# Performance work log

Measured on AMD Instinct MI355X. Metric: run time of the kernel, lower is better.

The kernel has to match this reference:

```python
import jax, jax.numpy as jnp
import numpy as np

N_NODES = 10000
N_EDGES = 320000
NODE_F = 64
EDGE_F = 32
H = 256
L = 6
HEADS = 8
OUT = H // HEADS
N_GRAPHS = 16
NEG_SLOPE = 0.2  # PyG GATConv leaky_relu slope


def setup_inputs() -> dict:
    key = jax.random.key(0)
    ks = jax.random.split(key, 32)
    s = 0.05
    f32 = jnp.float32
    inp = {}
    inp["x"] = jax.random.normal(ks[0], (N_NODES, NODE_F), f32)
    inp["edge_index"] = jax.random.randint(ks[1], (2, N_EDGES), 0, N_NODES)
    inp["edge_attr"] = jax.random.normal(ks[2], (N_EDGES, EDGE_F), f32)
    inp["batch"] = jnp.sort(jax.random.randint(ks[3], (N_NODES,), 0, N_GRAPHS))
    # embeddings
    inp["node_w"] = jax.random.normal(ks[4], (H, NODE_F), f32) * s
    inp["node_b"] = jnp.zeros((H,), f32)
    inp["edge_emb_w"] = jax.random.normal(ks[5], (H, EDGE_F), f32) * s
    inp["edge_emb_b"] = jnp.zeros((H,), f32)
    # stacked GATConv params (shared lin for src/dst since in_channels is int)
    inp["lin_w"] = jax.random.normal(ks[6], (L, H, H), f32) * s
    inp["att_src"] = jax.random.normal(ks[7], (L, HEADS, OUT), f32) * s
    inp["att_dst"] = jax.random.normal(ks[8], (L, HEADS, OUT), f32) * s
    inp["att_edge"] = jax.random.normal(ks[9], (L, HEADS, OUT), f32) * s
    inp["lin_edge_w"] = jax.random.normal(ks[10], (L, H, H), f32) * s
    inp["conv_b"] = jnp.zeros((L, H), f32)
    inp["ln_g"] = jnp.ones((L, H), f32)
    inp["ln_b"] = jnp.zeros((L, H), f32)
    # MLP heads: Linear(2H->H), Linear(H->H/2), Linear(H/2->3)
    inp["pw1"] = jax.random.normal(ks[11], (H, 2 * H), f32) * s
    inp["pb1"] = jnp.zeros((H,), f32)
    inp["pw2"] = jax.random.normal(ks[12], (H // 2, H), f32) * s
    inp["pb2"] = jnp.zeros((H // 2,), f32)
    inp["pw3"] = jax.random.normal(ks[13], (3, H // 2), f32) * s
    inp["pb3"] = jnp.zeros((3,), f32)
    inp["mw1"] = jax.random.normal(ks[14], (H, 2 * H), f32) * s
    inp["mb1"] = jnp.zeros((H,), f32)
    inp["mw2"] = jax.random.normal(ks[15], (H // 2, H), f32) * s
    inp["mb2"] = jnp.zeros((H // 2,), f32)
    inp["mw3"] = jax.random.normal(ks[16], (3, H // 2), f32) * s
    inp["mb3"] = jnp.zeros((3,), f32)
    return inp


def _ln(x, g, b):
    mu = jnp.mean(x, -1, keepdims=True)
    var = jnp.mean(jnp.square(x - mu), -1, keepdims=True)
    return g * (x - mu) * jax.lax.rsqrt(var + 1e-5) + b


def _mlp(z, w1, b1, w2, b2, w3, b3):
    h = jax.nn.gelu(z @ w1.T + b1, approximate=False)
    h = jax.nn.gelu(h @ w2.T + b2, approximate=False)
    return jax.nn.sigmoid(h @ w3.T + b3)


def _gnn_forward(x, edge_attr, src, dst, batch,
                 node_w, node_b, edge_emb_w, edge_emb_b,
                 lin_w, att_src, att_dst, att_edge, lin_edge_w, conv_b,
                 ln_g, ln_b,
                 pw1, pb1, pw2, pb2, pw3, pb3,
                 mw1, mb1, mw2, mb2, mw3, mb3):
    h = x @ node_w.T + node_b                       # [N, H]
    ea = edge_attr @ edge_emb_w.T + edge_emb_b      # [E, H]
    # PyG add_self_loops(fill_value='mean'): loop attr = mean of incoming edge attrs
    cnt = jax.ops.segment_sum(jnp.ones((N_EDGES,), h.dtype), dst, N_NODES)
    loop_attr = jax.ops.segment_sum(ea, dst, N_NODES) / jnp.maximum(cnt, 1.0)[:, None]
    ea_full = jnp.concatenate([ea, loop_attr], 0)   # [E+N, H]
    loops = jnp.arange(N_NODES, dtype=src.dtype)
    src_f = jnp.concatenate([src, loops])
    dst_f = jnp.concatenate([dst, loops])
    for i in range(L):
        x_in = h
        xw = (h @ lin_w[i].T).reshape(N_NODES, HEADS, OUT)
        eap = (ea_full @ lin_edge_w[i].T).reshape(-1, HEADS, OUT)
        a_src = jnp.sum(xw * att_src[i], -1)        # [N, heads]
        a_dst = jnp.sum(xw * att_dst[i], -1)
        alpha = a_src[src_f] + a_dst[dst_f] + jnp.sum(eap * att_edge[i], -1)  # [E+N, heads]
        alpha = jnp.where(alpha > 0, alpha, NEG_SLOPE * alpha)
        amax = jax.ops.segment_max(alpha, dst_f, N_NODES)
        e = jnp.exp(alpha - amax[dst_f])
        denom = jax.ops.segment_sum(e, dst_f, N_NODES)
        w = e / (denom[dst_f] + 1e-16)
        msg = xw[src_f] * w[:, :, None]             # [E+N, heads, out]
        hi = jax.ops.segment_sum(msg, dst_f, N_NODES).reshape(N_NODES, H) + conv_b[i]
        hi = jax.nn.gelu(_ln(hi, ln_g[i], ln_b[i]), approximate=False)
        h = hi + x_in if i > 0 else hi
    sums = jax.ops.segment_sum(h, batch, N_GRAPHS)  # [G, H]
    ncnt = jax.ops.segment_sum(jnp.ones((N_NODES,), h.dtype), batch, N_GRAPHS)
    mean = sums / jnp.maximum(ncnt, 1.0)[:, None]
    xg = jnp.concatenate([mean, sums], 1)           # [G, 2H]
    params = _mlp(xg, pw1, pb1, pw2, pb2, pw3, pb3)
    metrics = _mlp(xg, mw1, mb1, mw2, mb2, mw3, mb3)
    return params, metrics


def reference(x, edge_index, edge_attr, batch,
              node_w, node_b, edge_emb_w, edge_emb_b,
              lin_w, att_src, att_dst, att_edge, lin_edge_w, conv_b,
              ln_g, ln_b,
              pw1, pb1, pw2, pb2, pw3, pb3,
              mw1, mb1, mw2, mb2, mw3, mb3):
    return _gnn_forward(x, edge_attr, edge_index[0], edge_index[1], batch,
                        node_w, node_b, edge_emb_w, edge_emb_b,
                        lin_w, att_src, att_dst, att_edge, lin_edge_w, conv_b,
                        ln_g, ln_b,
                        pw1, pb1, pw2, pb2, pw3, pb3,
                        mw1, mb1, mw2, mb2, mw3, mb3)
```

## Files before the change

### kernel.cpp

```cpp
#include <hip/hip_runtime.h>
#include <math.h>

#define NN 10000
#define NE 320000
#define NODE_F 64
#define EDGE_F 32
#define HDIM 256
#define HEADS 8
#define LAYERS 6
#define NG 16
#define NPB 2
#define NOUT 48
#define LOG2E 1.4426950408889634f

typedef __attribute__((ext_vector_type(8))) short short8;
typedef __attribute__((ext_vector_type(4))) float float4v;
typedef __attribute__((ext_vector_type(2))) float floatx2;

__global__ void count_kernel(const int* __restrict__ dst, int* __restrict__ cnt) {
    int e = blockIdx.x * 256 + threadIdx.x;
    if (e < NE) atomicAdd(&cnt[dst[e]], 1);
}

__global__ void scan_kernel(const int* __restrict__ cnt, int* __restrict__ row_ptr,
                            int* __restrict__ pos) {
    __shared__ int wsum[16];
    __shared__ int woff[16];
    int t = threadIdx.x;
    int lane = t & 63, wid = t >> 6;
    const int chunk = 10;
    int lo = t * chunk;
    int loc[10];
    int s = 0;
    #pragma unroll
    for (int k = 0; k < 10; ++k) {
        int i = lo + k;
        int v = (i < NN) ? cnt[i] : 0;
        loc[k] = v;
        s += v;
    }
    int inc = s;
    #pragma unroll
    for (int off = 1; off < 64; off <<= 1) {
        int v = __shfl_up(inc, off, 64);
        if (lane >= off) inc += v;
    }
    if (lane == 63) wsum[wid] = inc;
    __syncthreads();
    if (t < 16) {
        int inc2 = wsum[t];
        #pragma unroll
        for (int off = 1; off < 16; off <<= 1) {
            int u = __shfl_up(inc2, off, 16);
            if (t >= off) inc2 += u;
        }
        woff[t] = inc2;
    }
    __syncthreads();
    int base = inc - s + (wid ? woff[wid - 1] : 0);
    #pragma unroll
    for (int k = 0; k < 10; ++k) {
        int i = lo + k;
        if (i < NN) {
            row_ptr[i] = base;
            pos[i] = base;
            base += loc[k];
        }
    }
    if (t == 1023) row_ptr[NN] = woff[15];
}

__global__ void scatter_kernel(const int* __restrict__ src, const int* __restrict__ dst,
                               int* __restrict__ pos, int2* __restrict__ csr_se) {
    int e = blockIdx.x * 256 + threadIdx.x;
    if (e >= NE) return;
    int d = dst[e];
    int idx = atomicAdd(&pos[d], 1);
    csr_se[idx] = make_int2(src[e], e);
}

__device__ __forceinline__ ushort f2bf(float f) {
    union { float f; unsigned u; } v; v.f = f;
    unsigned u = v.u;
    return (ushort)((u + 0x7fffu + ((u >> 16) & 1u)) >> 16);
}
__device__ __forceinline__ float bf2f(ushort b) {
    union { unsigned u; float f; } v; v.u = ((unsigned)b) << 16; return v.f;
}

__global__ __launch_bounds__(256) void prep_kernel(const float* __restrict__ att_edge,
                                                   const float* __restrict__ lin_edge_w,
                                                   const float* __restrict__ eew,
                                                   const float* __restrict__ eeb,
                                                   ushort* __restrict__ webbf,
                                                   float* __restrict__ bebuf) {
    int ih = blockIdx.x;
    int i = ih >> 3, h = ih & 7;
    __shared__ float vsh[HDIM];
    int t = threadIdx.x;
    float s = 0.f;
    const float* ae = att_edge + ih * 32;
    const float* lw = lin_edge_w + ((size_t)i * HDIM + h * 32) * HDIM + t;
    #pragma unroll
    for (int o = 0; o < 32; ++o) s += ae[o] * lw[(size_t)o * HDIM];
    vsh[t] = s;
    __syncthreads();
    if (t < EDGE_F) {
        float acc = 0.f;
        for (int k = 0; k < HDIM; ++k) acc += vsh[k] * eew[k * EDGE_F + t];
        webbf[ih * EDGE_F + t] = f2bf(acc * LOG2E);
    } else if (t == EDGE_F) {
        float acc = 0.f;
        for (int k = 0; k < HDIM; ++k) acc += vsh[k] * eeb[k];
        bebuf[ih] = acc * LOG2E;
    }
}

__global__ __launch_bounds__(256) void preE_kernel(const float* __restrict__ edge_attr,
                                                   const ushort* __restrict__ web,
                                                   const float* __restrict__ be,
                                                   ushort* __restrict__ preEb) {
    int wv = threadIdx.x >> 6, l = threadIdx.x & 63;
    int base = blockIdx.x * 64 + wv * 16;
    int m = l & 15, kq = (l >> 4) * 8;
    const float* ar = edge_attr + (size_t)(base + m) * EDGE_F + kq;
    float4 a0 = *(const float4*)(ar);
    float4 a1 = *(const float4*)(ar + 4);
    short8 afrag;
    afrag[0] = (short)f2bf(a0.x); afrag[1] = (short)f2bf(a0.y);
    afrag[2] = (short)f2bf(a0.z); afrag[3] = (short)f2bf(a0.w);
    afrag[4] = (short)f2bf(a1.x); afrag[5] = (short)f2bf(a1.y);
    afrag[6] = (short)f2bf(a1.z); afrag[7] = (short)f2bf(a1.w);
    float4v zero = {0.f, 0.f, 0.f, 0.f};
    float4v acc[3];
    #pragma unroll
    for (int ct = 0; ct < 3; ++ct) {
        short8 bfrag = *(const short8*)(web + (size_t)(ct * 16 + m) * EDGE_F + kq);
        acc[ct] = __builtin_amdgcn_mfma_f32_16x16x32_bf16(afrag, bfrag, zero, 0, 0, 0);
    }
    #pragma unroll
    for (int ct = 0; ct < 3; ++ct) {
        int oc = ct * 16 + m;
        int li = oc >> 3, hh = oc & 7;
        float bv = be[oc];
        #pragma unroll
        for (int r = 0; r < 4; ++r) {
            int row = (l >> 4) * 4 + r;
            preEb[(size_t)li * NE * 8 + (size_t)(base + row) * 8 + hh] = f2bf(acc[ct][r] + bv);
        }
    }
}

__global__ void tobf_all_kernel(const float* __restrict__ lin_w, const float* __restrict__ node_w,
                                const float* __restrict__ x, ushort* __restrict__ wbhi,
                                ushort* __restrict__ nwhi, ushort* __restrict__ xhi) {
    const int N1 = LAYERS * HDIM * HDIM;
    const int N2 = N1 + HDIM * NODE_F;
    const int N3 = N2 + NN * NODE_F;
    int i = blockIdx.x * 256 + threadIdx.x;
    if (i < N1) wbhi[i] = f2bf(lin_w[i]);
    else if (i < N2) nwhi[i - N1] = f2bf(node_w[i - N1]);
    else if (i < N3) xhi[i - N2] = f2bf(x[i - N2]);
}

__global__ __launch_bounds__(128) void gemm_bf1(const ushort* __restrict__ Ah,
                                                const ushort* __restrict__ Bh,
                                                const float* __restrict__ bias,
                                                float* __restrict__ C,
                                                ushort* __restrict__ Chi,
                                                unsigned char* __restrict__ Cf8,
                                                const float* __restrict__ att_s,
                                                const float* __restrict__ att_d,
                                                float* __restrict__ a_src,
                                                float* __restrict__ a_dst,
                                                int N, int K, int J) {
    __shared__ ushort sAh[64][40], sBh[64][40];
    int nb = blockIdx.y * 64, jb = blockIdx.x * 64;
    int t = threadIdx.x, w = t >> 6, l = t & 63;
    int srow = t >> 1, sq = (t & 1) * 16;
    int fr = l & 15, fq = (l >> 4) * 8;
    float4v acc[2][4] = {};
    for (int kt = 0; kt < K; kt += 32) {
        int gr = nb + srow;
        short8 a0 = {0,0,0,0,0,0,0,0}, a1 = {0,0,0,0,0,0,0,0};
        if (gr < N) {
            const short8* pa = (const short8*)(Ah + (size_t)gr * K + kt + sq);
            a0 = pa[0]; a1 = pa[1];
        }
        *(short8*)&sAh[srow][sq] = a0; *(short8*)&sAh[srow][sq + 8] = a1;
        const short8* pb = (const short8*)(Bh + (size_t)(jb + srow) * K + kt + sq);
        short8 b0 = pb[0], b1 = pb[1];
        *(short8*)&sBh[srow][sq] = b0; *(short8*)&sBh[srow][sq + 8] = b1;
        __syncthreads();
        short8 bh[4];
        #pragma unroll
        for (int nt = 0; nt < 4; ++nt)
            bh[nt] = *(const short8*)&sBh[nt * 16 + fr][fq];
        #pragma unroll
        for (int mt = 0; mt < 2; ++mt) {
            short8 ah = *(const short8*)&sAh[w * 32 + mt * 16 + fr][fq];
            #pragma unroll
            for (int nt = 0; nt < 4; ++nt)
                acc[mt][nt] = __builtin_amdgcn_mfma_f32_16x16x32_bf16(ah, bh[nt], acc[mt][nt], 0, 0, 0);
        }
        __syncthreads();
    }
    #pragma unroll
    for (int mt = 0; mt < 2; ++mt) {
        #pragma unroll
        for (int nt = 0; nt < 4; ++nt) {
            int col = jb + nt * 16 + fr;
            float bv = bias ? bias[col] : 0.f;
            #pragma unroll
            for (int r = 0; r < 4; ++r) {
                int row = nb + w * 32 + mt * 16 + (l >> 4) * 4 + r;
                if (row < N) {
                    float v = acc[mt][nt][r] + bv;
                    if (C) C[(size_t)row * J + col] = v;
                    if (Chi) Chi[(size_t)row * J + col] = f2bf(v);
                    if (Cf8) {
                        int pk8 = __builtin_amdgcn_cvt_pk_fp8_f32(v, v, 0, false);
                        Cf8[(size_t)row * J + col] = (unsigned char)(pk8 & 0xff);
                    }
                }
            }
        }
    }
    if (att_s) {
        int head0 = jb >> 5;
        float cs[4], cd[4];
        #pragma unroll
        for (int nt = 0; nt < 4; ++nt) {
            cs[nt] = att_s[jb + nt * 16 + fr] * LOG2E;
            cd[nt] = att_d[jb + nt * 16 + fr] * LOG2E;
        }
        #pragma unroll
        for (int mt = 0; mt < 2; ++mt) {
            #pragma unroll
            for (int r = 0; r < 4; ++r) {
                float s0 = acc[mt][0][r] * cs[0] + acc[mt][1][r] * cs[1];
                float s1 = acc[mt][2][r] * cs[2] + acc[mt][3][r] * cs[3];
                float d0 = acc[mt][0][r] * cd[0] + acc[mt][1][r] * cd[1];
                float d1 = acc[mt][2][r] * cd[2] + acc[mt][3][r] * cd[3];
                #pragma unroll
                for (int off = 8; off >= 1; off >>= 1) {
                    s0 += __shfl_xor(s0, off, 16);
                    s1 += __shfl_xor(s1, off, 16);
                    d0 += __shfl_xor(d0, off, 16);
                    d1 += __shfl_xor(d1, off, 16);
                }
                if (fr == 0) {
                    int row = nb + w * 32 + mt * 16 + (l >> 4) * 4 + r;
                    if (row < N) {
                        a_src[row * 8 + head0]     = s0;
                        a_src[row * 8 + head0 + 1] = s1;
                        a_dst[row * 8 + head0]     = d0;
                        a_dst[row * 8 + head0 + 1] = d1;
                    }
                }
            }
        }
    }
}

__device__ __forceinline__ float gelu_exact(float x) {
    return 0.5f * x * (1.f + erff(x * 0.70710678118654752f));
}

__global__ __launch_bounds__(64 * NPB) void node_kernel(const unsigned char* __restrict__ xwf8,
                                                  const ushort* __restrict__ pb,
                                                  const float* __restrict__ a_src,
                                                  const float* __restrict__ a_dst,
                                                  const int* __restrict__ row_ptr,
                                                  const int2* __restrict__ csr_se,
                                                  const float* __restrict__ h_prev,
                                                  float* __restrict__ h_next,
                                                  ushort* __restrict__ hhi,
                                                  const float* __restrict__ cb,
                                                  const float* __restrict__ lg,
                                                  const float* __restrict__ lb, int first) {
    int wv = threadIdx.x >> 6, l = threadIdx.x & 63;
    int n = blockIdx.x * NPB + wv;
    int start = row_ptr[n], end = row_ptr[n + 1];
    int hc = l >> 3;
    int hc8 = l & 56;
    int jj = l & 7;
    float adnh = a_dst[n * 8 + hc];
    const unsigned char* xb = xwf8 + 4 * l;

    float den = 0.f, acc[4] = {0.f, 0.f, 0.f, 0.f};
    float psum = 0.f;
    for (int idx = start; idx < end; idx += 8) {
        int myi = idx + jj;
        bool valid = myi < end;
        int2 se = valid ? csr_se[myi] : make_int2(n, 0);
        int snj[8];
        #pragma unroll
        for (int j = 0; j < 8; ++j) snj[j] = __shfl(se.x, hc8 + j, 64);
        unsigned g[8];
        #pragma unroll
        for (int j = 0; j < 8; ++j) g[j] = *(const unsigned*)(xb + (size_t)snj[j] * HDIM);
        float w_t = 0.f;
        if (valid) {
            float p_t = bf2f(pb[(size_t)se.y * 8 + hc]);
            float a_t = a_src[(size_t)se.x * 8 + hc] + adnh + p_t;
            w_t = exp2f(fminf(fmaxf(a_t, 0.2f * a_t), 57.7f));
            psum += p_t;
        }
        #pragma unroll
        for (int j = 0; j < 8; ++j) {
            float wj = __shfl(w_t, hc8 + j, 64);
            floatx2 lo = __builtin_amdgcn_cvt_pk_f32_fp8(g[j], false);
            floatx2 hi = __builtin_amdgcn_cvt_pk_f32_fp8(g[j], true);
            den += wj;
            acc[0] += wj * lo.x;
            acc[1] += wj * lo.y;
            acc[2] += wj * hi.x;
            acc[3] += wj * hi.y;
        }
    }
    #pragma unroll
    for (int off = 1; off < 8; off <<= 1) psum += __shfl_xor(psum, off, 64);
    int deg = end - start;
    float preLv = deg > 0 ? psum / (float)deg : 0.f;
    {
        float al = a_src[n * 8 + hc] + adnh + preLv;
        al = fminf(fmaxf(al, 0.2f * al), 57.7f);
        float wself = exp2f(al);
        den += wself;
        unsigned gs = *(const unsigned*)(xb + (size_t)n * HDIM);
        floatx2 lo = __builtin_amdgcn_cvt_pk_f32_fp8(gs, false);
        floatx2 hi = __builtin_amdgcn_cvt_pk_f32_fp8(gs, true);
        acc[0] += wself * lo.x;
        acc[1] += wself * lo.y;
        acc[2] += wself * hi.x;
        acc[3] += wself * hi.y;
    }
    float4 cb4 = *(const float4*)(cb + 4 * l);
    float invh = 1.f / (den + 1e-16f);
    acc[0] = acc[0] * invh + cb4.x;
    acc[1] = acc[1] * invh + cb4.y;
    acc[2] = acc[2] * invh + cb4.z;
    acc[3] = acc[3] * invh + cb4.w;

    float part = acc[0] + acc[1] + acc[2] + acc[3];
    #pragma unroll
    for (int off = 32; off >= 1; off >>= 1) part += __shfl_xor(part, off, 64);
    float mu = part * (1.f / 256.f);
    float p2 = 0.f;
    #pragma unroll
    for (int j = 0; j < 4; ++j) {
        float d = acc[j] - mu;
        p2 += d * d;
    }
    #pragma unroll
    for (int off = 32; off >= 1; off >>= 1) p2 += __shfl_xor(p2, off, 64);
    float rstd = rsqrtf(p2 * (1.f / 256.f) + 1e-5f);

    float4 lg4 = *(const float4*)(lg + 4 * l);
    float4 lb4 = *(const float4*)(lb + 4 * l);
    float o4[4];
    float lgv[4] = {lg4.x, lg4.y, lg4.z, lg4.w};
    float lbv[4] = {lb4.x, lb4.y, lb4.z, lb4.w};
    float4 hp = make_float4(0.f, 0.f, 0.f, 0.f);
    if (!first) hp = *(const float4*)(h_prev + (size_t)n * HDIM + 4 * l);
    float hpv[4] = {hp.x, hp.y, hp.z, hp.w};
    #pragma unroll
    for (int j = 0; j < 4; ++j) {
        float y = (acc[j] - mu) * rstd * lgv[j] + lbv[j];
        o4[j] = gelu_exact(y) + hpv[j];
    }
    *(float4*)(h_next + (size_t)n * HDIM + 4 * l) = make_float4(o4[0], o4[1], o4[2], o4[3]);
    if (hhi) {
        uint2 ph;
        ph.x = (unsigned)f2bf(o4[0]) | ((unsigned)f2bf(o4[1]) << 16);
        ph.y = (unsigned)f2bf(o4[2]) | ((unsigned)f2bf(o4[3]) << 16);
        *(uint2*)(hhi + (size_t)n * HDIM + 4 * l) = ph;
    }
}

__global__ __launch_bounds__(256) void graph_sum_kernel(const float* __restrict__ h,
                                                        const int* __restrict__ batch,
                                                        float* __restrict__ sums) {
    int t = threadIdx.x;
    int n0 = blockIdx.x * 64;
    int n1 = min(NN, n0 + 64);
    float acc = 0.f;
    int cur = batch[n0];
    for (int n = n0; n < n1; ++n) {
        int b = batch[n];
        if (b != cur) {
            atomicAdd(&sums[cur * HDIM + t], acc);
            acc = 0.f;
            cur = b;
        }
        acc += h[(size_t)n * HDIM + t];
    }
    atomicAdd(&sums[cur * HDIM + t], acc);
}

__device__ __forceinline__ int lower_bound_dev(const int* a, int n, int v) {
    int lo = 0, hi = n;
    while (lo < hi) {
        int mid = (lo + hi) >> 1;
        if (a[mid] < v) lo = mid + 1; else hi = mid;
    }
    return lo;
}

__global__ __launch_bounds__(256) void mlp_kernel(const float* __restrict__ sums,
                                                  const int* __restrict__ batch,
                                                  const float* __restrict__ pw1,
                                                  const float* __restrict__ pb1,
                                                  const float* __restrict__ pw2,
                                                  const float* __restrict__ pb2,
                                                  const float* __restrict__ pw3,
                                                  const float* __restrict__ pb3,
                                                  const float* __restrict__ mw1,
                                                  const float* __restrict__ mb1,
                                                  const float* __restrict__ mw2,
                                                  const float* __restrict__ mb2,
                                                  const float* __restrict__ mw3,
                                                  const float* __restrict__ mb3,
                                                  float* __restrict__ out) {
    int g = blockIdx.x, which = blockIdx.y;
    const float* w1 = which ? mw1 : pw1; const float* b1 = which ? mb1 : pb1;
    const float* w2 = which ? mw2 : pw2; const float* b2 = which ? mb2 : pb2;
    const float* w3 = which ? mw3 : pw3; const float* b3 = which ? mb3 : pb3;
    __shared__ float xg[512];
    __shared__ float h1[256];
    __shared__ float h2[128];
    __shared__ float cinv_s;
    int t = threadIdx.x;
    if (t == 0) {
        int s0 = lower_bound_dev(batch, NN, g), s1 = lower_bound_dev(batch, NN, g + 1);
        cinv_s = 1.f / fmaxf((float)(s1 - s0), 1.f);
    }
    __syncthreads();
    float sv = sums[g * HDIM + t];
    xg[t] = sv * cinv_s;
    xg[256 + t] = sv;
    __syncthreads();
    {
        const float* wr = w1 + (size_t)t * 512;
        float acc = 0.f;
        #pragma unroll 8
        for (int k = 0; k < 512; k += 4) {
            float4 wv = *(const float4*)(wr + k);
            acc += wv.x * xg[k] + wv.y * xg[k + 1] + wv.z * xg[k + 2] + wv.w * xg[k + 3];
        }
        h1[t] = gelu_exact(acc + b1[t]);
    }
    __syncthreads();
    {
        int row = t >> 1, hf = t & 1;
        const float* wr = w2 + (size_t)row * 256 + hf * 128;
        const float* hx = h1 + hf * 128;
        float acc = 0.f;
        #pragma unroll 8
        for (int k = 0; k < 128; k += 4) {
            float4 wv = *(const float4*)(wr + k);
            acc += wv.x * hx[k] + wv.y * hx[k + 1] + wv.z * hx[k + 2] + wv.w * hx[k + 3];
        }
        acc += __shfl_xor(acc, 1, 64);
        if (hf == 0) h2[row] = gelu_exact(acc + b2[row]);
    }
    __syncthreads();
    if (t < 64) {
        float v0 = h2[t], v1 = h2[64 + t];
        #pragma unroll
        for (int o = 0; o < 3; ++o) {
            float p = w3[o * 128 + t] * v0 + w3[o * 128 + 64 + t] * v1;
            #pragma unroll
            for (int off = 32; off >= 1; off >>= 1) p += __shfl_xor(p, off, 64);
            if (t == 0) out[which * (NG * 3) + g * 3 + o] = 1.f / (1.f + expf(-(p + b3[o])));
        }
    }
}

extern "C" void kernel_launch(void* const* d_in, const int* in_sizes, int n_in, void* d_out,
                              int out_size, void* d_ws, size_t ws_size, hipStream_t stream) {
    const float* x         = (const float*)d_in[0];
    const int*   ei        = (const int*)d_in[1];
    const int*   src       = ei;
    const int*   dst       = ei + NE;
    const float* edge_attr = (const float*)d_in[2];
    const int*   batch     = (const int*)d_in[3];
    const float* node_w    = (const float*)d_in[4];
    const float* node_b    = (const float*)d_in[5];
    const float* eew       = (const float*)d_in[6];
    const float* eeb       = (const float*)d_in[7];
    const float* lin_w     = (const float*)d_in[8];
    const float* att_src   = (const float*)d_in[9];
    const float* att_dst   = (const float*)d_in[10];
    const float* att_edge  = (const float*)d_in[11];
    const float* lin_edge_w= (const float*)d_in[12];
    const float* conv_b    = (const float*)d_in[13];
    const float* ln_g      = (const float*)d_in[14];
    const float* ln_b      = (const float*)d_in[15];
    const float* pw1 = (const float*)d_in[16]; const float* pb1 = (const float*)d_in[17];
    const float* pw2 = (const float*)d_in[18]; const float* pb2 = (const float*)d_in[19];
    const float* pw3 = (const float*)d_in[20]; const float* pb3 = (const float*)d_in[21];
    const float* mw1 = (const float*)d_in[22]; const float* mb1 = (const float*)d_in[23];
    const float* mw2 = (const float*)d_in[24]; const float* mb2 = (const float*)d_in[25];
    const float* mw3 = (const float*)d_in[26]; const float* mb3 = (const float*)d_in[27];
    float* out = (float*)d_out;

    float* wsf = (float*)d_ws;
    float* hA        = wsf; wsf += (size_t)NN * HDIM;
    float* hB        = wsf; wsf += (size_t)NN * HDIM;
    float* a_src     = wsf; wsf += (size_t)NN * HEADS;
    float* a_dst     = wsf; wsf += (size_t)NN * HEADS;
    float* bebuf     = wsf; wsf += 64;
    ushort* ubuf = (ushort*)wsf;
    ushort* preEb = ubuf; ubuf += (size_t)NE * NOUT;
    ushort* webbf = ubuf; ubuf += (size_t)NOUT * EDGE_F;
    ushort* hhi  = ubuf; ubuf += (size_t)NN * HDIM;
    unsigned char* xwf8 = (unsigned char*)ubuf; ubuf += (size_t)NN * HDIM / 2;
    ushort* wbhi = ubuf; ubuf += (size_t)LAYERS * HDIM * HDIM;
    ushort* xhi  = ubuf; ubuf += (size_t)NN * NODE_F;
    ushort* nwhi = ubuf; ubuf += (size_t)HDIM * NODE_F;
    int* ibuf    = (int*)ubuf;
    int* cnt     = ibuf; ibuf += NN + 16;
    float* sums  = (float*)ibuf; ibuf += NG * HDIM;
    int* row_ptr = ibuf; ibuf += NN + 16;
    int* pos     = ibuf; ibuf += NN + 16;
    ibuf += (((size_t)ibuf & 4) ? 1 : 0);
    int2* csr_se = (int2*)ibuf; ibuf += 2 * NE;

    hipMemsetAsync(cnt, 0, (NN + 16 + NG * HDIM) * sizeof(int), stream);
    count_kernel<<<(NE + 255) / 256, 256, 0, stream>>>(dst, cnt);
    scan_kernel<<<1, 1024, 0, stream>>>(cnt, row_ptr, pos);
    scatter_kernel<<<(NE + 255) / 256, 256, 0, stream>>>(src, dst, pos, csr_se);

    prep_kernel<<<LAYERS * HEADS, 256, 0, stream>>>(att_edge, lin_edge_w, eew, eeb, webbf, bebuf);
    preE_kernel<<<NE / 64, 256, 0, stream>>>(edge_attr, webbf, bebuf, preEb);

    {
        const int total = LAYERS * HDIM * HDIM + HDIM * NODE_F + NN * NODE_F;
        tobf_all_kernel<<<(total + 255) / 256, 256, 0, stream>>>(lin_w, node_w, x,
                                                                 wbhi, nwhi, xhi);
    }

    {
        dim3 grid(HDIM / 64, (NN + 63) / 64);
        gemm_bf1<<<grid, 128, 0, stream>>>(xhi, nwhi, node_b, nullptr, hhi, nullptr,
                                           nullptr, nullptr, nullptr, nullptr,
                                           NN, NODE_F, HDIM);
    }

    float* cur = hA;
    float* nxt = hB;
    for (int i = 0; i < LAYERS; ++i) {
        dim3 grid(HDIM / 64, (NN + 63) / 64);
        gemm_bf1<<<grid, 128, 0, stream>>>(hhi, wbhi + (size_t)i * HDIM * HDIM, nullptr,
                                           nullptr, nullptr, xwf8,
                                           att_src + i * HEADS * 32, att_dst + i * HEADS * 32,
                                           a_src, a_dst, NN, HDIM, HDIM);
        node_kernel<<<NN / NPB, 64 * NPB, 0, stream>>>(
            xwf8, preEb + (size_t)i * NE * 8, a_src, a_dst,
            row_ptr, csr_se, cur, nxt, (i == LAYERS - 1) ? nullptr : hhi,
            conv_b + i * HDIM, ln_g + i * HDIM, ln_b + i * HDIM, i == 0 ? 1 : 0);
        float* tmp = cur; cur = nxt; nxt = tmp;
    }

    graph_sum_kernel<<<(NN + 63) / 64, 256, 0, stream>>>(cur, batch, sums);
    {
        dim3 gm(NG, 2);
        mlp_kernel<<<gm, 256, 0, stream>>>(sums, batch, pw1, pb1, pw2, pb2, pw3, pb3,
                                           mw1, mb1, mw2, mb2, mw3, mb3, out);
    }
}
```

Measured before the change: 509.1 us.

## Unroll edge gather loop by 16 and fuse graph pooling into last node kernel

The per-node attention aggregation loop now handles two groups of 8 edges per iteration. This issues 16 fp8 row gathers before any arithmetic, so more memory loads are in flight per wave. In the last layer, the node kernel atomically adds its outputs into per-graph sums instead of writing h. That removes the separate graph_sum kernel and one full read of the hidden state. The trade-off is more register pressure in the unrolled loop and heavy float atomic contention on 16 graph rows, plus a non-deterministic summation order.

```diff
diff --git a/kernel.cpp b/kernel.cpp
--- a/kernel.cpp
+++ b/kernel.cpp
@@ -278,7 +278,9 @@
                                                   ushort* __restrict__ hhi,
                                                   const float* __restrict__ cb,
                                                   const float* __restrict__ lg,
-                                                  const float* __restrict__ lb, int first) {
+                                                  const float* __restrict__ lb, int first,
+                                                  const int* __restrict__ batch,
+                                                  float* __restrict__ sums) {
     int wv = threadIdx.x >> 6, l = threadIdx.x & 63;
     int n = blockIdx.x * NPB + wv;
     int start = row_ptr[n], end = row_ptr[n + 1];
@@ -290,28 +292,52 @@
 
     float den = 0.f, acc[4] = {0.f, 0.f, 0.f, 0.f};
     float psum = 0.f;
-    for (int idx = start; idx < end; idx += 8) {
-        int myi = idx + jj;
-        bool valid = myi < end;
-        int2 se = valid ? csr_se[myi] : make_int2(n, 0);
-        int snj[8];
-        #pragma unroll
-        for (int j = 0; j < 8; ++j) snj[j] = __shfl(se.x, hc8 + j, 64);
-        unsigned g[8];
-        #pragma unroll
-        for (int j = 0; j < 8; ++j) g[j] = *(const unsigned*)(xb + (size_t)snj[j] * HDIM);
-        float w_t = 0.f;
-        if (valid) {
-            float p_t = bf2f(pb[(size_t)se.y * 8 + hc]);
-            float a_t = a_src[(size_t)se.x * 8 + hc] + adnh + p_t;
-            w_t = exp2f(fminf(fmaxf(a_t, 0.2f * a_t), 57.7f));
+    for (int idx = start; idx < end; idx += 16) {
+        int myi0 = idx + jj;
+        int myi1 = idx + 8 + jj;
+        bool v0 = myi0 < end;
+        bool v1 = myi1 < end;
+        int2 se0 = v0 ? csr_se[myi0] : make_int2(n, 0);
+        int2 se1 = v1 ? csr_se[myi1] : make_int2(n, 0);
+        int snj0[8], snj1[8];
+        #pragma unroll
+        for (int j = 0; j < 8; ++j) snj0[j] = __shfl(se0.x, hc8 + j, 64);
+        #pragma unroll
+        for (int j = 0; j < 8; ++j) snj1[j] = __shfl(se1.x, hc8 + j, 64);
+        unsigned g0[8], g1[8];
+        #pragma unroll
+        for (int j = 0; j < 8; ++j) g0[j] = *(const unsigned*)(xb + (size_t)snj0[j] * HDIM);
+        #pragma unroll
+        for (int j = 0; j < 8; ++j) g1[j] = *(const unsigned*)(xb + (size_t)snj1[j] * HDIM);
+        float w0 = 0.f, w1 = 0.f;
+        if (v0) {
+            float p_t = bf2f(pb[(size_t)se0.y * 8 + hc]);
+            float a_t = a_src[(size_t)se0.x * 8 + hc] + adnh + p_t;
+            w0 = exp2f(fminf(fmaxf(a_t, 0.2f * a_t), 57.7f));
             psum += p_t;
         }
+        if (v1) {
+            float p_t = bf2f(pb[(size_t)se1.y * 8 + hc]);
+            float a_t = a_src[(size_t)se1.x * 8 + hc] + adnh + p_t;
+            w1 = exp2f(fminf(fmaxf(a_t, 0.2f * a_t), 57.7f));
+            psum += p_t;
+        }
         #pragma unroll
         for (int j = 0; j < 8; ++j) {
-            float wj = __shfl(w_t, hc8 + j, 64);
-            floatx2 lo = __builtin_amdgcn_cvt_pk_f32_fp8(g[j], false);
-            floatx2 hi = __builtin_amdgcn_cvt_pk_f32_fp8(g[j], true);
+            float wj = __shfl(w0, hc8 + j, 64);
+            floatx2 lo = __builtin_amdgcn_cvt_pk_f32_fp8(g0[j], false);
+            floatx2 hi = __builtin_amdgcn_cvt_pk_f32_fp8(g0[j], true);
+            den += wj;
+            acc[0] += wj * lo.x;
+            acc[1] += wj * lo.y;
+            acc[2] += wj * hi.x;
+            acc[3] += wj * hi.y;
+        }
+        #pragma unroll
+        for (int j = 0; j < 8; ++j) {
+            float wj = __shfl(w1, hc8 + j, 64);
+            floatx2 lo = __builtin_amdgcn_cvt_pk_f32_fp8(g1[j], false);
+            floatx2 hi = __builtin_amdgcn_cvt_pk_f32_fp8(g1[j], true);
             den += wj;
             acc[0] += wj * lo.x;
             acc[1] += wj * lo.y;
@@ -370,33 +396,22 @@
         float y = (acc[j] - mu) * rstd * lgv[j] + lbv[j];
         o4[j] = gelu_exact(y) + hpv[j];
     }
-    *(float4*)(h_next + (size_t)n * HDIM + 4 * l) = make_float4(o4[0], o4[1], o4[2], o4[3]);
+    if (sums) {
+        int b = batch[n];
+        float* sp = sums + (size_t)b * HDIM + 4 * l;
+        atomicAdd(sp + 0, o4[0]);
+        atomicAdd(sp + 1, o4[1]);
+        atomicAdd(sp + 2, o4[2]);
+        atomicAdd(sp + 3, o4[3]);
+    } else {
+        *(float4*)(h_next + (size_t)n * HDIM + 4 * l) = make_float4(o4[0], o4[1], o4[2], o4[3]);
+    }
     if (hhi) {
         uint2 ph;
         ph.x = (unsigned)f2bf(o4[0]) | ((unsigned)f2bf(o4[1]) << 16);
         ph.y = (unsigned)f2bf(o4[2]) | ((unsigned)f2bf(o4[3]) << 16);
         *(uint2*)(hhi + (size_t)n * HDIM + 4 * l) = ph;
     }
-}
-
-__global__ __launch_bounds__(256) void graph_sum_kernel(const float* __restrict__ h,
-                                                        const int* __restrict__ batch,
-                                                        float* __restrict__ sums) {
-    int t = threadIdx.x;
-    int n0 = blockIdx.x * 64;
-    int n1 = min(NN, n0 + 64);
-    float acc = 0.f;
-    int cur = batch[n0];
-    for (int n = n0; n < n1; ++n) {
-        int b = batch[n];
-        if (b != cur) {
-            atomicAdd(&sums[cur * HDIM + t], acc);
-            acc = 0.f;
-            cur = b;
-        }
-        acc += h[(size_t)n * HDIM + t];
-    }
-    atomicAdd(&sums[cur * HDIM + t], acc);
 }
 
 __device__ __forceinline__ int lower_bound_dev(const int* a, int n, int v) {
@@ -525,7 +540,6 @@
     float* sums  = (float*)ibuf; ibuf += NG * HDIM;
     int* row_ptr = ibuf; ibuf += NN + 16;
     int* pos     = ibuf; ibuf += NN + 16;
-    ibuf += (((size_t)ibuf & 4) ? 1 : 0);
     int2* csr_se = (int2*)ibuf; ibuf += 2 * NE;
 
     hipMemsetAsync(cnt, 0, (NN + 16 + NG * HDIM) * sizeof(int), stream);
@@ -557,14 +571,15 @@
                                            nullptr, nullptr, xwf8,
                                            att_src + i * HEADS * 32, att_dst + i * HEADS * 32,
                                            a_src, a_dst, NN, HDIM, HDIM);
+        int last = (i == LAYERS - 1);
         node_kernel<<<NN / NPB, 64 * NPB, 0, stream>>>(
             xwf8, preEb + (size_t)i * NE * 8, a_src, a_dst,
-            row_ptr, csr_se, cur, nxt, (i == LAYERS - 1) ? nullptr : hhi,
-            conv_b + i * HDIM, ln_g + i * HDIM, ln_b + i * HDIM, i == 0 ? 1 : 0);
+            row_ptr, csr_se, cur, nxt, last ? nullptr : hhi,
+            conv_b + i * HDIM, ln_g + i * HDIM, ln_b + i * HDIM, i == 0 ? 1 : 0,
+            batch, last ? sums : nullptr);
         float* tmp = cur; cur = nxt; nxt = tmp;
     }
 
-    graph_sum_kernel<<<(NN + 63) / 64, 256, 0, stream>>>(cur, batch, sums);
     {
         dim3 gm(NG, 2);
         mlp_kernel<<<gm, 256, 0, stream>>>(sums, batch, pw1, pb1, pw2, pb2, pw3, pb3,
```

Measured after the change: 629.0 us. 1.24x slower.

## Fold node embedding into first GAT linear and keep hidden state in bf16

Applied to the files above, without the earlier changes.

Precomputes the product of the first layer's lin_w with the node embedding weight and bias, so layer 0's projection runs as one K=64 GEMM straight from x and the separate embedding GEMM is dropped. The hidden state is also kept only in bf16 ping-pong buffers instead of fp32 plus a bf16 copy. This cuts fp32 reads and writes of the residual in every node_kernel and in graph_sum. The cost is lower residual precision, since bf16 rounding accumulates across layers.

```diff
diff --git a/kernel.cpp b/kernel.cpp
--- a/kernel.cpp
+++ b/kernel.cpp
@@ -114,6 +114,26 @@
         for (int k = 0; k < HDIM; ++k) acc += vsh[k] * eeb[k];
         bebuf[ih] = acc * LOG2E;
     }
+}
+
+__global__ __launch_bounds__(64) void fold0_kernel(const float* __restrict__ lin_w,
+                                                   const float* __restrict__ node_w,
+                                                   const float* __restrict__ node_b,
+                                                   ushort* __restrict__ w0p,
+                                                   float* __restrict__ b0p) {
+    int j = blockIdx.x, f = threadIdx.x;
+    const float* wr = lin_w + (size_t)j * HDIM;
+    float acc = 0.f, accb = 0.f;
+    for (int k = 0; k < HDIM; ++k) acc += wr[k] * node_w[k * NODE_F + f];
+    #pragma unroll
+    for (int m = 0; m < 4; ++m) {
+        int k = f + 64 * m;
+        accb += wr[k] * node_b[k];
+    }
+    w0p[j * NODE_F + f] = f2bf(acc);
+    #pragma unroll
+    for (int off = 32; off >= 1; off >>= 1) accb += __shfl_xor(accb, off, 64);
+    if (f == 0) b0p[j] = accb;
 }
 
 __global__ __launch_bounds__(256) void preE_kernel(const float* __restrict__ edge_attr,
@@ -151,29 +171,25 @@
     }
 }
 
-__global__ void tobf_all_kernel(const float* __restrict__ lin_w, const float* __restrict__ node_w,
+__global__ void tobf_all_kernel(const float* __restrict__ lin_w,
                                 const float* __restrict__ x, ushort* __restrict__ wbhi,
-                                ushort* __restrict__ nwhi, ushort* __restrict__ xhi) {
+                                ushort* __restrict__ xhi) {
     const int N1 = LAYERS * HDIM * HDIM;
-    const int N2 = N1 + HDIM * NODE_F;
-    const int N3 = N2 + NN * NODE_F;
+    const int N2 = N1 + NN * NODE_F;
     int i = blockIdx.x * 256 + threadIdx.x;
     if (i < N1) wbhi[i] = f2bf(lin_w[i]);
-    else if (i < N2) nwhi[i - N1] = f2bf(node_w[i - N1]);
-    else if (i < N3) xhi[i - N2] = f2bf(x[i - N2]);
+    else if (i < N2) xhi[i - N1] = f2bf(x[i - N1]);
 }
 
 __global__ __launch_bounds__(128) void gemm_bf1(const ushort* __restrict__ Ah,
                                                 const ushort* __restrict__ Bh,
                                                 const float* __restrict__ bias,
-                                                float* __restrict__ C,
-                                                ushort* __restrict__ Chi,
                                                 unsigned char* __restrict__ Cf8,
                                                 const float* __restrict__ att_s,
                                                 const float* __restrict__ att_d,
                                                 float* __restrict__ a_src,
                                                 float* __restrict__ a_dst,
-                                                int N, int K, int J) {
+                                                int N, int K) {
     __shared__ ushort sAh[64][40], sBh[64][40];
     int nb = blockIdx.y * 64, jb = blockIdx.x * 64;
     int t = threadIdx.x, w = t >> 6, l = t & 63;
@@ -205,28 +221,33 @@
         }
         __syncthreads();
     }
+    if (bias) {
+        #pragma unroll
+        for (int nt = 0; nt < 4; ++nt) {
+            float bv = bias[jb + nt * 16 + fr];
+            #pragma unroll
+            for (int mt = 0; mt < 2; ++mt)
+                #pragma unroll
+                for (int r = 0; r < 4; ++r) acc[mt][nt][r] += bv;
+        }
+    }
     #pragma unroll
     for (int mt = 0; mt < 2; ++mt) {
         #pragma unroll
         for (int nt = 0; nt < 4; ++nt) {
             int col = jb + nt * 16 + fr;
-            float bv = bias ? bias[col] : 0.f;
             #pragma unroll
             for (int r = 0; r < 4; ++r) {
                 int row = nb + w * 32 + mt * 16 + (l >> 4) * 4 + r;
                 if (row < N) {
-                    float v = acc[mt][nt][r] + bv;
-                    if (C) C[(size_t)row * J + col] = v;
-                    if (Chi) Chi[(size_t)row * J + col] = f2bf(v);
-                    if (Cf8) {
-                        int pk8 = __builtin_amdgcn_cvt_pk_fp8_f32(v, v, 0, false);
-                        Cf8[(size_t)row * J + col] = (unsigned char)(pk8 & 0xff);
-                    }
+                    float v = acc[mt][nt][r];
+                    int pk8 = __builtin_amdgcn_cvt_pk_fp8_f32(v, v, 0, false);
+                    Cf8[(size_t)row * HDIM + col] = (unsigned char)(pk8 & 0xff);
                 }
             }
         }
     }
-    if (att_s) {
+    {
         int head0 = jb >> 5;
         float cs[4], cd[4];
         #pragma unroll
@@ -273,9 +294,8 @@
                                                   const float* __restrict__ a_dst,
                                                   const int* __restrict__ row_ptr,
                                                   const int2* __restrict__ csr_se,
-                                                  const float* __restrict__ h_prev,
-                                                  float* __restrict__ h_next,
-                                                  ushort* __restrict__ hhi,
+                                                  const ushort* __restrict__ hp,
+                                                  ushort* __restrict__ hout,
                                                   const float* __restrict__ cb,
                                                   const float* __restrict__ lg,
                                                   const float* __restrict__ lb, int first) {
@@ -362,24 +382,26 @@
     float o4[4];
     float lgv[4] = {lg4.x, lg4.y, lg4.z, lg4.w};
     float lbv[4] = {lb4.x, lb4.y, lb4.z, lb4.w};
-    float4 hp = make_float4(0.f, 0.f, 0.f, 0.f);
-    if (!first) hp = *(const float4*)(h_prev + (size_t)n * HDIM + 4 * l);
-    float hpv[4] = {hp.x, hp.y, hp.z, hp.w};
+    float hpv[4] = {0.f, 0.f, 0.f, 0.f};
+    if (!first) {
+        uint2 ph = *(const uint2*)(hp + (size_t)n * HDIM + 4 * l);
+        hpv[0] = bf2f((ushort)(ph.x & 0xffff));
+        hpv[1] = bf2f((ushort)(ph.x >> 16));
+        hpv[2] = bf2f((ushort)(ph.y & 0xffff));
+        hpv[3] = bf2f((ushort)(ph.y >> 16));
+    }
     #pragma unroll
     for (int j = 0; j < 4; ++j) {
         float y = (acc[j] - mu) * rstd * lgv[j] + lbv[j];
         o4[j] = gelu_exact(y) + hpv[j];
     }
-    *(float4*)(h_next + (size_t)n * HDIM + 4 * l) = make_float4(o4[0], o4[1], o4[2], o4[3]);
-    if (hhi) {
-        uint2 ph;
-        ph.x = (unsigned)f2bf(o4[0]) | ((unsigned)f2bf(o4[1]) << 16);
-        ph.y = (unsigned)f2bf(o4[2]) | ((unsigned)f2bf(o4[3]) << 16);
-        *(uint2*)(hhi + (size_t)n * HDIM + 4 * l) = ph;
-    }
-}
-
-__global__ __launch_bounds__(256) void graph_sum_kernel(const float* __restrict__ h,
+    uint2 po;
+    po.x = (unsigned)f2bf(o4[0]) | ((unsigned)f2bf(o4[1]) << 16);
+    po.y = (unsigned)f2bf(o4[2]) | ((unsigned)f2bf(o4[3]) << 16);
+    *(uint2*)(hout + (size_t)n * HDIM + 4 * l) = po;
+}
+
+__global__ __launch_bounds__(256) void graph_sum_kernel(const ushort* __restrict__ h,
                                                         const int* __restrict__ batch,
                                                         float* __restrict__ sums) {
     int t = threadIdx.x;
@@ -394,7 +416,7 @@
             acc = 0.f;
             cur = b;
         }
-        acc += h[(size_t)n * HDIM + t];
+        acc += bf2f(h[(size_t)n * HDIM + t]);
     }
     atomicAdd(&sums[cur * HDIM + t], acc);
 }
@@ -507,25 +529,24 @@
     float* out = (float*)d_out;
 
     float* wsf = (float*)d_ws;
-    float* hA        = wsf; wsf += (size_t)NN * HDIM;
-    float* hB        = wsf; wsf += (size_t)NN * HDIM;
     float* a_src     = wsf; wsf += (size_t)NN * HEADS;
     float* a_dst     = wsf; wsf += (size_t)NN * HEADS;
     float* bebuf     = wsf; wsf += 64;
+    float* b0p       = wsf; wsf += HDIM;
     ushort* ubuf = (ushort*)wsf;
     ushort* preEb = ubuf; ubuf += (size_t)NE * NOUT;
     ushort* webbf = ubuf; ubuf += (size_t)NOUT * EDGE_F;
-    ushort* hhi  = ubuf; ubuf += (size_t)NN * HDIM;
+    ushort* hb0  = ubuf; ubuf += (size_t)NN * HDIM;
+    ushort* hb1  = ubuf; ubuf += (size_t)NN * HDIM;
     unsigned char* xwf8 = (unsigned char*)ubuf; ubuf += (size_t)NN * HDIM / 2;
     ushort* wbhi = ubuf; ubuf += (size_t)LAYERS * HDIM * HDIM;
     ushort* xhi  = ubuf; ubuf += (size_t)NN * NODE_F;
-    ushort* nwhi = ubuf; ubuf += (size_t)HDIM * NODE_F;
+    ushort* w0p  = ubuf; ubuf += (size_t)HDIM * NODE_F;
     int* ibuf    = (int*)ubuf;
     int* cnt     = ibuf; ibuf += NN + 16;
     float* sums  = (float*)ibuf; ibuf += NG * HDIM;
     int* row_ptr = ibuf; ibuf += NN + 16;
     int* pos     = ibuf; ibuf += NN + 16;
-    ibuf += (((size_t)ibuf & 4) ? 1 : 0);
     int2* csr_se = (int2*)ibuf; ibuf += 2 * NE;
 
     hipMemsetAsync(cnt, 0, (NN + 16 + NG * HDIM) * sizeof(int), stream);
@@ -537,34 +558,28 @@
     preE_kernel<<<NE / 64, 256, 0, stream>>>(edge_attr, webbf, bebuf, preEb);
 
     {
-        const int total = LAYERS * HDIM * HDIM + HDIM * NODE_F + NN * NODE_F;
-        tobf_all_kernel<<<(total + 255) / 256, 256, 0, stream>>>(lin_w, node_w, x,
-                                                                 wbhi, nwhi, xhi);
-    }
-
-    {
-        dim3 grid(HDIM / 64, (NN + 63) / 64);
-        gemm_bf1<<<grid, 128, 0, stream>>>(xhi, nwhi, node_b, nullptr, hhi, nullptr,
-                                           nullptr, nullptr, nullptr, nullptr,
-                                           NN, NODE_F, HDIM);
-    }
-
-    float* cur = hA;
-    float* nxt = hB;
+        const int total = LAYERS * HDIM * HDIM + NN * NODE_F;
+        tobf_all_kernel<<<(total + 255) / 256, 256, 0, stream>>>(lin_w, x, wbhi, xhi);
+    }
+    fold0_kernel<<<HDIM, 64, 0, stream>>>(lin_w, node_w, node_b, w0p, b0p);
+
+    ushort* hb[2] = {hb0, hb1};
     for (int i = 0; i < LAYERS; ++i) {
         dim3 grid(HDIM / 64, (NN + 63) / 64);
-        gemm_bf1<<<grid, 128, 0, stream>>>(hhi, wbhi + (size_t)i * HDIM * HDIM, nullptr,
-                                           nullptr, nullptr, xwf8,
+        const ushort* Ain = (i == 0) ? xhi : hb[(i - 1) & 1];
+        const ushort* Bin = (i == 0) ? w0p : wbhi + (size_t)i * HDIM * HDIM;
+        int Kin = (i == 0) ? NODE_F : HDIM;
+        const float* bias = (i == 0) ? b0p : nullptr;
+        gemm_bf1<<<grid, 128, 0, stream>>>(Ain, Bin, bias, xwf8,
                                            att_src + i * HEADS * 32, att_dst + i * HEADS * 32,
-                                           a_src, a_dst, NN, HDIM, HDIM);
+                                           a_src, a_dst, NN, Kin);
         node_kernel<<<NN / NPB, 64 * NPB, 0, stream>>>(
             xwf8, preEb + (size_t)i * NE * 8, a_src, a_dst,
-            row_ptr, csr_se, cur, nxt, (i == LAYERS - 1) ? nullptr : hhi,
+            row_ptr, csr_se, (i == 0) ? nullptr : hb[(i - 1) & 1], hb[i & 1],
             conv_b + i * HDIM, ln_g + i * HDIM, ln_b + i * HDIM, i == 0 ? 1 : 0);
-        float* tmp = cur; cur = nxt; nxt = tmp;
-    }
-
-    graph_sum_kernel<<<(NN + 63) / 64, 256, 0, stream>>>(cur, batch, sums);
+    }
+
+    graph_sum_kernel<<<(NN + 63) / 64, 256, 0, stream>>>(hb[(LAYERS - 1) & 1], batch, sums);
     {
         dim3 gm(NG, 2);
         mlp_kernel<<<gm, 256, 0, stream>>>(sums, batch, pw1, pb1, pw2, pb2, pw3, pb3,
```

Result: faster. 477.3 us (-6.3%).
